# Kernel tuning notes

Measured on AMD Instinct MI355X. Metric: run time of the kernel, lower is better.

## Reference

```python
import jax, jax.numpy as jnp
import numpy as np

WEIGHT = 1e-7       # lambda for the CRF loss
SIGMA_RGB = 15.0    # color-similarity bandwidth
SIGMA_XY = 100.0    # spatial-proximity bandwidth
SCALE = 0.5         # scale_factor (sigma_xy is multiplied by it in forward)


def setup_inputs() -> dict:
    key = jax.random.key(0)
    k1, k2 = jax.random.split(key)
    images = jax.random.uniform(k1, (4, 3, 128, 128), jnp.float32) * 255.0  # [0,255] RGB
    logits = jax.random.normal(k2, (4, 4, 128, 128), jnp.float32)
    segmentations = jax.nn.softmax(logits, axis=1)  # softmaxed logits, N*K*H*W
    return {"images": images, "segmentations": segmentations}


def _crf_loss(images, segmentations):
    n, k, h, w = segmentations.shape
    # F.interpolate(images, scale_factor=0.5, mode='nearest') == stride-2 subsample
    img_s = images[:, :, ::2, ::2]
    # F.interpolate(segs, scale_factor=0.5, mode='bilinear', align_corners=False)
    # for exact /2 downscale == 2x2 average pooling
    hs, ws = h // 2, w // 2
    seg_s = segmentations.reshape(n, k, hs, 2, ws, 2).mean(axis=(3, 5))  # [n,k,hs,ws]

    P = hs * ws
    yy, xx = jnp.meshgrid(jnp.arange(hs, dtype=jnp.float32),
                          jnp.arange(ws, dtype=jnp.float32), indexing='ij')
    sigma_xy_eff = SIGMA_XY * SCALE
    pos = jnp.stack([xx, yy], axis=-1).reshape(P, 2) / sigma_xy_eff      # [P,2]
    rgb = img_s.reshape(n, 3, P).transpose(0, 2, 1) / SIGMA_RGB          # [n,P,3]
    feats = jnp.concatenate([jnp.broadcast_to(pos[None], (n, P, 2)), rgb], axis=-1)  # [n,P,5]

    # exact dense Gaussian bilateral kernel W_ij = exp(-0.5*||f_i - f_j||^2)
    sq = jnp.sum(feats * feats, axis=-1)                                 # [n,P]
    d2 = sq[:, :, None] + sq[:, None, :] - 2.0 * jnp.einsum('npc,nqc->npq', feats, feats)
    Wk = jnp.exp(-0.5 * jnp.maximum(d2, 0.0))                            # [n,P,P]

    S = seg_s.reshape(n, k, P)
    AS = jnp.einsum('npq,nkq->nkp', Wk, S)                               # bilateral-filtered segs
    loss = -jnp.sum(S * AS) / jnp.float32(n)
    return (WEIGHT * loss).reshape(1)


def reference(images, segmentations):
    return _crf_loss(images, segmentations)
```

## Files before the change

kernel.cpp:

```cpp
#include <hip/hip_runtime.h>

#define NB   4
#define KCH  4
#define PPB  4096
#define QT   64
#define BLK  256
#define PT   2
#define NPT  8
#define NBLK 288

#if __has_builtin(__builtin_amdgcn_exp2f)
#define EXPFN(x) __builtin_amdgcn_exp2f(x)
#define FSCALE 1.2011224087864498f
#else
#define EXPFN(x) __expf(x)
#define FSCALE 1.0f
#endif


__global__ __launch_bounds__(256) void crf_prep(const float* __restrict__ images,
                                                const float* __restrict__ segs,
                                                float4* __restrict__ RA,
                                                float4* __restrict__ RB,
                                                float2* __restrict__ RC) {
    int gid = blockIdx.x * BLK + threadIdx.x;
    int n = gid >> 12;
    int p = gid & (PPB - 1);
    int i = p >> 6;
    int j = p & 63;
    int off = 256 * i + 2 * j;
    const float* img = images + (size_t)n * 3 * 16384;
    float x = (float)j * (FSCALE / 50.0f);
    float y = (float)i * (FSCALE / 50.0f);
    float r = img[off]         * (FSCALE / 15.0f);
    float g = img[16384 + off] * (FSCALE / 15.0f);
    float b = img[32768 + off] * (FSCALE / 15.0f);
    float h = -0.5f * (x * x + y * y + r * r + g * g + b * b);
    const float* sg = segs + (size_t)n * KCH * 16384;
    float s0, s1, s2, s3;
    {
        float2 u0 = *(const float2*)(sg + off);
        float2 u1 = *(const float2*)(sg + off + 128);
        s0 = 0.25f * ((u0.x + u0.y) + (u1.x + u1.y));
        u0 = *(const float2*)(sg + 16384 + off);
        u1 = *(const float2*)(sg + 16384 + off + 128);
        s1 = 0.25f * ((u0.x + u0.y) + (u1.x + u1.y));
        u0 = *(const float2*)(sg + 32768 + off);
        u1 = *(const float2*)(sg + 32768 + off + 128);
        s2 = 0.25f * ((u0.x + u0.y) + (u1.x + u1.y));
        u0 = *(const float2*)(sg + 49152 + off);
        u1 = *(const float2*)(sg + 49152 + off + 128);
        s3 = 0.25f * ((u0.x + u0.y) + (u1.x + u1.y));
    }
    RA[gid] = make_float4(x, y, r, g);
    RB[gid] = make_float4(b, h, s0, s1);
    RC[gid] = make_float2(s2, s3);
}

__global__ __launch_bounds__(256) void crf_pairs(const float4* __restrict__ RA,
                                                 const float4* __restrict__ RB,
                                                 const float2* __restrict__ RC,
                                                 float* __restrict__ out) {
    __shared__ float wsum[BLK / 64];
    int t = threadIdx.x;
    int n = blockIdx.y;

    int b = blockIdx.x;
    int pt = 0;
    pt += (b >= 64); pt += (b >= 120); pt += (b >= 168); pt += (b >= 208);
    pt += (b >= 240); pt += (b >= 264); pt += (b >= 280);
    int qc = b - pt * (60 - 4 * pt);
    int pbase = pt * (BLK * PT);
    int qbase = qc * QT;
    bool mixed = (qc >> 3) == pt;
    int base = n << 12;

    float4 a0 = RA[base + pbase + t];
    float4 a1 = RA[base + pbase + t + BLK];
    float4 b0 = RB[base + pbase + t];
    float4 b1 = RB[base + pbase + t + BLK];
    float2 c0 = RC[base + pbase + t];
    float2 c1 = RC[base + pbase + t + BLK];

    const float4* __restrict__ qA = RA + base + qbase;
    const float4* __restrict__ qB = RB + base + qbase;
    const float2* __restrict__ qC = RC + base + qbase;

    float acc0 = 0.f, acc1 = 0.f;
    float acc_all;

    if (!mixed) {
#pragma unroll 4
        for (int q = 0; q < QT; ++q) {
            float4 fa = qA[q];
            float4 fb = qB[q];
            float2 fc = qC[q];
            float d0 = b0.y + fb.y;
            d0 = fmaf(a0.x, fa.x, d0);
            d0 = fmaf(a0.y, fa.y, d0);
            d0 = fmaf(a0.z, fa.z, d0);
            d0 = fmaf(a0.w, fa.w, d0);
            d0 = fmaf(b0.x, fb.x, d0);
            float w0 = EXPFN(d0);
            float sd0 = b0.z * fb.z;
            sd0 = fmaf(b0.w, fb.w, sd0);
            sd0 = fmaf(c0.x, fc.x, sd0);
            sd0 = fmaf(c0.y, fc.y, sd0);
            acc0 = fmaf(w0, sd0, acc0);

            float d1 = b1.y + fb.y;
            d1 = fmaf(a1.x, fa.x, d1);
            d1 = fmaf(a1.y, fa.y, d1);
            d1 = fmaf(a1.z, fa.z, d1);
            d1 = fmaf(a1.w, fa.w, d1);
            d1 = fmaf(b1.x, fb.x, d1);
            float w1 = EXPFN(d1);
            float sd1 = b1.z * fb.z;
            sd1 = fmaf(b1.w, fb.w, sd1);
            sd1 = fmaf(c1.x, fc.x, sd1);
            sd1 = fmaf(c1.y, fc.y, sd1);
            acc1 = fmaf(w1, sd1, acc1);
        }
        acc_all = 2.0f * (acc0 + acc1);
    } else {
        int pg0 = pbase + t;
        int pg1 = pbase + t + BLK;
#pragma unroll 4
        for (int q = 0; q < QT; ++q) {
            float4 fa = qA[q];
            float4 fb = qB[q];
            float2 fc = qC[q];
            int qg = qbase + q;

            float d0 = b0.y + fb.y;
            d0 = fmaf(a0.x, fa.x, d0);
            d0 = fmaf(a0.y, fa.y, d0);
            d0 = fmaf(a0.z, fa.z, d0);
            d0 = fmaf(a0.w, fa.w, d0);
            d0 = fmaf(b0.x, fb.x, d0);
            float w0 = EXPFN(d0);
            float sd0 = b0.z * fb.z;
            sd0 = fmaf(b0.w, fb.w, sd0);
            sd0 = fmaf(c0.x, fc.x, sd0);
            sd0 = fmaf(c0.y, fc.y, sd0);
            float f0 = (qg > pg0) ? 2.0f : ((qg == pg0) ? 1.0f : 0.0f);
            acc0 = fmaf(w0, sd0 * f0, acc0);

            float d1 = b1.y + fb.y;
            d1 = fmaf(a1.x, fa.x, d1);
            d1 = fmaf(a1.y, fa.y, d1);
            d1 = fmaf(a1.z, fa.z, d1);
            d1 = fmaf(a1.w, fa.w, d1);
            d1 = fmaf(b1.x, fb.x, d1);
            float w1 = EXPFN(d1);
            float sd1 = b1.z * fb.z;
            sd1 = fmaf(b1.w, fb.w, sd1);
            sd1 = fmaf(c1.x, fc.x, sd1);
            sd1 = fmaf(c1.y, fc.y, sd1);
            float f1 = (qg > pg1) ? 2.0f : ((qg == pg1) ? 1.0f : 0.0f);
            acc1 = fmaf(w1, sd1 * f1, acc1);
        }
        acc_all = acc0 + acc1;
    }

#pragma unroll
    for (int off = 32; off > 0; off >>= 1)
        acc_all += __shfl_down(acc_all, off, 64);
    if ((t & 63) == 0) wsum[t >> 6] = acc_all;
    __syncthreads();
    if (t == 0) {
        float s = (wsum[0] + wsum[1]) + (wsum[2] + wsum[3]);
        atomicAdd(out, s * (-2.5e-8f));
    }
}

extern "C" void kernel_launch(void* const* d_in, const int* in_sizes, int n_in,
                              void* d_out, int out_size, void* d_ws, size_t ws_size,
                              hipStream_t stream) {
    const float* images = (const float*)d_in[0];
    const float* segs   = (const float*)d_in[1];
    float* out = (float*)d_out;
    char* ws = (char*)d_ws;
    float4* RA = (float4*)(ws);
    float4* RB = (float4*)(ws + 262144);
    float2* RC = (float2*)(ws + 524288);
    (void)in_sizes; (void)n_in; (void)out_size; (void)ws_size;

    (void)hipMemsetAsync(out, 0, sizeof(float), stream);
    crf_prep<<<dim3(64), dim3(256), 0, stream>>>(images, segs, RA, RB, RC);
    crf_pairs<<<dim3(NBLK, NB), dim3(256), 0, stream>>>(RA, RB, RC, out);
}
```

Baseline: 78.90 us.

## Stage q-tile in LDS, raise pixels per thread to four, fold memset into prep

Each thread now holds four p-pixels in registers instead of two. The 64-entry q tile is staged once into shared memory and software-prefetched one step ahead. The triangular block schedule is recomputed for 160 blocks per image, and the separate memset of the output is replaced by a store in the prep kernel. The aims are more work per q-feature load, one fewer launch, and replacing repeated global loads with LDS broadcasts. In exchange there are fewer blocks per image (640 total), which may underfill the GPU, and the four accumulators raise register pressure.

```diff
diff --git a/kernel.cpp b/kernel.cpp
--- a/kernel.cpp
+++ b/kernel.cpp
@@ -5,9 +5,8 @@
 #define PPB  4096
 #define QT   64
 #define BLK  256
-#define PT   2
-#define NPT  8
-#define NBLK 288
+#define PT   4
+#define NBLK 160
 
 #if __has_builtin(__builtin_amdgcn_exp2f)
 #define EXPFN(x) __builtin_amdgcn_exp2f(x)
@@ -22,8 +21,10 @@
                                                 const float* __restrict__ segs,
                                                 float4* __restrict__ RA,
                                                 float4* __restrict__ RB,
-                                                float2* __restrict__ RC) {
+                                                float2* __restrict__ RC,
+                                                float* __restrict__ out) {
     int gid = blockIdx.x * BLK + threadIdx.x;
+    if (gid == 0) out[0] = 0.0f;
     int n = gid >> 12;
     int p = gid & (PPB - 1);
     int i = p >> 6;
@@ -61,106 +62,95 @@
                                                  const float4* __restrict__ RB,
                                                  const float2* __restrict__ RC,
                                                  float* __restrict__ out) {
+    __shared__ float4 ldsA[QT + 1];
+    __shared__ float4 ldsB[QT + 1];
+    __shared__ float2 ldsC[QT + 1];
     __shared__ float wsum[BLK / 64];
+
     int t = threadIdx.x;
     int n = blockIdx.y;
 
     int b = blockIdx.x;
-    int pt = 0;
-    pt += (b >= 64); pt += (b >= 120); pt += (b >= 168); pt += (b >= 208);
-    pt += (b >= 240); pt += (b >= 264); pt += (b >= 280);
-    int qc = b - pt * (60 - 4 * pt);
+    int pt = (b >= 64) + (b >= 112) + (b >= 144);
+    int qc = b - 8 * pt * (7 - pt);
     int pbase = pt * (BLK * PT);
     int qbase = qc * QT;
-    bool mixed = (qc >> 3) == pt;
+    bool mixed = (qc >> 4) == pt;
     int base = n << 12;
 
-    float4 a0 = RA[base + pbase + t];
-    float4 a1 = RA[base + pbase + t + BLK];
-    float4 b0 = RB[base + pbase + t];
-    float4 b1 = RB[base + pbase + t + BLK];
-    float2 c0 = RC[base + pbase + t];
-    float2 c1 = RC[base + pbase + t + BLK];
+    if (t < QT)            ldsA[t]          = RA[base + qbase + t];
+    else if (t < 2 * QT)   ldsB[t - QT]     = RB[base + qbase + (t - QT)];
+    else if (t < 3 * QT)   ldsC[t - 2 * QT] = RC[base + qbase + (t - 2 * QT)];
 
-    const float4* __restrict__ qA = RA + base + qbase;
-    const float4* __restrict__ qB = RB + base + qbase;
-    const float2* __restrict__ qC = RC + base + qbase;
+    float4 pa[PT], pb[PT];
+    float2 pc[PT];
+#pragma unroll
+    for (int pi = 0; pi < PT; ++pi) {
+        int idx = base + pbase + t + pi * BLK;
+        pa[pi] = RA[idx];
+        pb[pi] = RB[idx];
+        pc[pi] = RC[idx];
+    }
+    __syncthreads();
 
-    float acc0 = 0.f, acc1 = 0.f;
+    float acc[PT] = {0.f, 0.f, 0.f, 0.f};
     float acc_all;
 
+    float4 fa = ldsA[0];
+    float4 fb = ldsB[0];
+    float2 fc = ldsC[0];
+
     if (!mixed) {
-#pragma unroll 4
+#pragma unroll 2
         for (int q = 0; q < QT; ++q) {
-            float4 fa = qA[q];
-            float4 fb = qB[q];
-            float2 fc = qC[q];
-            float d0 = b0.y + fb.y;
-            d0 = fmaf(a0.x, fa.x, d0);
-            d0 = fmaf(a0.y, fa.y, d0);
-            d0 = fmaf(a0.z, fa.z, d0);
-            d0 = fmaf(a0.w, fa.w, d0);
-            d0 = fmaf(b0.x, fb.x, d0);
-            float w0 = EXPFN(d0);
-            float sd0 = b0.z * fb.z;
-            sd0 = fmaf(b0.w, fb.w, sd0);
-            sd0 = fmaf(c0.x, fc.x, sd0);
-            sd0 = fmaf(c0.y, fc.y, sd0);
-            acc0 = fmaf(w0, sd0, acc0);
-
-            float d1 = b1.y + fb.y;
-            d1 = fmaf(a1.x, fa.x, d1);
-            d1 = fmaf(a1.y, fa.y, d1);
-            d1 = fmaf(a1.z, fa.z, d1);
-            d1 = fmaf(a1.w, fa.w, d1);
-            d1 = fmaf(b1.x, fb.x, d1);
-            float w1 = EXPFN(d1);
-            float sd1 = b1.z * fb.z;
-            sd1 = fmaf(b1.w, fb.w, sd1);
-            sd1 = fmaf(c1.x, fc.x, sd1);
-            sd1 = fmaf(c1.y, fc.y, sd1);
-            acc1 = fmaf(w1, sd1, acc1);
+            float4 na = ldsA[q + 1];
+            float4 nb = ldsB[q + 1];
+            float2 nc = ldsC[q + 1];
+#pragma unroll
+            for (int pi = 0; pi < PT; ++pi) {
+                float d = pb[pi].y + fb.y;
+                d = fmaf(pa[pi].x, fa.x, d);
+                d = fmaf(pa[pi].y, fa.y, d);
+                d = fmaf(pa[pi].z, fa.z, d);
+                d = fmaf(pa[pi].w, fa.w, d);
+                d = fmaf(pb[pi].x, fb.x, d);
+                float w = EXPFN(d);
+                float sd = pb[pi].z * fb.z;
+                sd = fmaf(pb[pi].w, fb.w, sd);
+                sd = fmaf(pc[pi].x, fc.x, sd);
+                sd = fmaf(pc[pi].y, fc.y, sd);
+                acc[pi] = fmaf(w, sd, acc[pi]);
+            }
+            fa = na; fb = nb; fc = nc;
         }
-        acc_all = 2.0f * (acc0 + acc1);
+        acc_all = 2.0f * ((acc[0] + acc[1]) + (acc[2] + acc[3]));
     } else {
-        int pg0 = pbase + t;
-        int pg1 = pbase + t + BLK;
-#pragma unroll 4
+#pragma unroll 2
         for (int q = 0; q < QT; ++q) {
-            float4 fa = qA[q];
-            float4 fb = qB[q];
-            float2 fc = qC[q];
+            float4 na = ldsA[q + 1];
+            float4 nb = ldsB[q + 1];
+            float2 nc = ldsC[q + 1];
             int qg = qbase + q;
-
-            float d0 = b0.y + fb.y;
-            d0 = fmaf(a0.x, fa.x, d0);
-            d0 = fmaf(a0.y, fa.y, d0);
-            d0 = fmaf(a0.z, fa.z, d0);
-            d0 = fmaf(a0.w, fa.w, d0);
-            d0 = fmaf(b0.x, fb.x, d0);
-            float w0 = EXPFN(d0);
-            float sd0 = b0.z * fb.z;
-            sd0 = fmaf(b0.w, fb.w, sd0);
-            sd0 = fmaf(c0.x, fc.x, sd0);
-            sd0 = fmaf(c0.y, fc.y, sd0);
-            float f0 = (qg > pg0) ? 2.0f : ((qg == pg0) ? 1.0f : 0.0f);
-            acc0 = fmaf(w0, sd0 * f0, acc0);
-
-            float d1 = b1.y + fb.y;
-            d1 = fmaf(a1.x, fa.x, d1);
-            d1 = fmaf(a1.y, fa.y, d1);
-            d1 = fmaf(a1.z, fa.z, d1);
-            d1 = fmaf(a1.w, fa.w, d1);
-            d1 = fmaf(b1.x, fb.x, d1);
-            float w1 = EXPFN(d1);
-            float sd1 = b1.z * fb.z;
-            sd1 = fmaf(b1.w, fb.w, sd1);
-            sd1 = fmaf(c1.x, fc.x, sd1);
-            sd1 = fmaf(c1.y, fc.y, sd1);
-            float f1 = (qg > pg1) ? 2.0f : ((qg == pg1) ? 1.0f : 0.0f);
-            acc1 = fmaf(w1, sd1 * f1, acc1);
+#pragma unroll
+            for (int pi = 0; pi < PT; ++pi) {
+                int pg = pbase + t + pi * BLK;
+                float d = pb[pi].y + fb.y;
+                d = fmaf(pa[pi].x, fa.x, d);
+                d = fmaf(pa[pi].y, fa.y, d);
+                d = fmaf(pa[pi].z, fa.z, d);
+                d = fmaf(pa[pi].w, fa.w, d);
+                d = fmaf(pb[pi].x, fb.x, d);
+                float w = EXPFN(d);
+                float sd = pb[pi].z * fb.z;
+                sd = fmaf(pb[pi].w, fb.w, sd);
+                sd = fmaf(pc[pi].x, fc.x, sd);
+                sd = fmaf(pc[pi].y, fc.y, sd);
+                float f = (qg > pg) ? 2.0f : ((qg == pg) ? 1.0f : 0.0f);
+                acc[pi] = fmaf(w, sd * f, acc[pi]);
+            }
+            fa = na; fb = nb; fc = nc;
         }
-        acc_all = acc0 + acc1;
+        acc_all = (acc[0] + acc[1]) + (acc[2] + acc[3]);
     }
 
 #pragma unroll
@@ -186,7 +176,6 @@
     float2* RC = (float2*)(ws + 524288);
     (void)in_sizes; (void)n_in; (void)out_size; (void)ws_size;
 
-    (void)hipMemsetAsync(out, 0, sizeof(float), stream);
-    crf_prep<<<dim3(64), dim3(256), 0, stream>>>(images, segs, RA, RB, RC);
+    crf_prep<<<dim3(64), dim3(256), 0, stream>>>(images, segs, RA, RB, RC, out);
     crf_pairs<<<dim3(NBLK, NB), dim3(256), 0, stream>>>(RA, RB, RC, out);
 }
```

Measured after the change: 77.78 us. No clear change (-1.4%).

## Halve q-tile, stage q features in LDS, replace atomics with two-pass reduction

Applied to the files above, without the earlier changes.

Cuts the q tile from 64 to 32 so the triangular pair grid has twice as many blocks (576 per image), which spreads the exp-heavy work across more CUs. Each block now stages its q-point features in shared memory instead of reading them from global memory per iteration. The per-block atomicAdd and the memset are replaced by a partial-sum buffer and a separate single-block reduction kernel. This adds one extra kernel launch and a barrier per block.

```diff
diff --git a/kernel.cpp b/kernel.cpp
--- a/kernel.cpp
+++ b/kernel.cpp
@@ -3,11 +3,11 @@
 #define NB   4
 #define KCH  4
 #define PPB  4096
-#define QT   64
+#define QT   32
 #define BLK  256
 #define PT   2
-#define NPT  8
-#define NBLK 288
+#define NBLK 576
+#define NPART (NBLK * NB)
 
 #if __has_builtin(__builtin_amdgcn_exp2f)
 #define EXPFN(x) __builtin_amdgcn_exp2f(x)
@@ -57,34 +57,39 @@
     RC[gid] = make_float2(s2, s3);
 }
 
-__global__ __launch_bounds__(256) void crf_pairs(const float4* __restrict__ RA,
-                                                 const float4* __restrict__ RB,
-                                                 const float2* __restrict__ RC,
-                                                 float* __restrict__ out) {
+__global__ __launch_bounds__(256, 8) void crf_pairs(const float4* __restrict__ RA,
+                                                    const float4* __restrict__ RB,
+                                                    const float2* __restrict__ RC,
+                                                    float* __restrict__ part) {
+    __shared__ float4 ldsA[QT];
+    __shared__ float4 ldsB[QT];
+    __shared__ float2 ldsC[QT];
     __shared__ float wsum[BLK / 64];
+
     int t = threadIdx.x;
     int n = blockIdx.y;
 
     int b = blockIdx.x;
     int pt = 0;
-    pt += (b >= 64); pt += (b >= 120); pt += (b >= 168); pt += (b >= 208);
-    pt += (b >= 240); pt += (b >= 264); pt += (b >= 280);
-    int qc = b - pt * (60 - 4 * pt);
+#pragma unroll
+    for (int i = 1; i < 8; ++i) pt += (b >= 8 * i * (17 - i)) ? 1 : 0;
+    int qc = b - 8 * pt * (17 - pt) + 16 * pt;
     int pbase = pt * (BLK * PT);
     int qbase = qc * QT;
-    bool mixed = (qc >> 3) == pt;
+    bool mixed = (qc >> 4) == pt;
     int base = n << 12;
 
-    float4 a0 = RA[base + pbase + t];
-    float4 a1 = RA[base + pbase + t + BLK];
-    float4 b0 = RB[base + pbase + t];
-    float4 b1 = RB[base + pbase + t + BLK];
-    float2 c0 = RC[base + pbase + t];
-    float2 c1 = RC[base + pbase + t + BLK];
-
-    const float4* __restrict__ qA = RA + base + qbase;
-    const float4* __restrict__ qB = RB + base + qbase;
-    const float2* __restrict__ qC = RC + base + qbase;
+    if (t < QT)            ldsA[t]          = RA[base + qbase + t];
+    else if (t < 2 * QT)   ldsB[t - QT]     = RB[base + qbase + (t - QT)];
+    else if (t < 3 * QT)   ldsC[t - 2 * QT] = RC[base + qbase + (t - 2 * QT)];
+
+    float4 pa0 = RA[base + pbase + t];
+    float4 pa1 = RA[base + pbase + t + BLK];
+    float4 pb0 = RB[base + pbase + t];
+    float4 pb1 = RB[base + pbase + t + BLK];
+    float2 pc0 = RC[base + pbase + t];
+    float2 pc1 = RC[base + pbase + t + BLK];
+    __syncthreads();
 
     float acc0 = 0.f, acc1 = 0.f;
     float acc_all;
@@ -92,33 +97,33 @@
     if (!mixed) {
 #pragma unroll 4
         for (int q = 0; q < QT; ++q) {
-            float4 fa = qA[q];
-            float4 fb = qB[q];
-            float2 fc = qC[q];
-            float d0 = b0.y + fb.y;
-            d0 = fmaf(a0.x, fa.x, d0);
-            d0 = fmaf(a0.y, fa.y, d0);
-            d0 = fmaf(a0.z, fa.z, d0);
-            d0 = fmaf(a0.w, fa.w, d0);
-            d0 = fmaf(b0.x, fb.x, d0);
+            float4 fa = ldsA[q];
+            float4 fb = ldsB[q];
+            float2 fc = ldsC[q];
+            float d0 = pb0.y + fb.y;
+            d0 = fmaf(pa0.x, fa.x, d0);
+            d0 = fmaf(pa0.y, fa.y, d0);
+            d0 = fmaf(pa0.z, fa.z, d0);
+            d0 = fmaf(pa0.w, fa.w, d0);
+            d0 = fmaf(pb0.x, fb.x, d0);
             float w0 = EXPFN(d0);
-            float sd0 = b0.z * fb.z;
-            sd0 = fmaf(b0.w, fb.w, sd0);
-            sd0 = fmaf(c0.x, fc.x, sd0);
-            sd0 = fmaf(c0.y, fc.y, sd0);
+            float sd0 = pb0.z * fb.z;
+            sd0 = fmaf(pb0.w, fb.w, sd0);
+            sd0 = fmaf(pc0.x, fc.x, sd0);
+            sd0 = fmaf(pc0.y, fc.y, sd0);
             acc0 = fmaf(w0, sd0, acc0);
 
-            float d1 = b1.y + fb.y;
-            d1 = fmaf(a1.x, fa.x, d1);
-            d1 = fmaf(a1.y, fa.y, d1);
-            d1 = fmaf(a1.z, fa.z, d1);
-            d1 = fmaf(a1.w, fa.w, d1);
-            d1 = fmaf(b1.x, fb.x, d1);
+            float d1 = pb1.y + fb.y;
+            d1 = fmaf(pa1.x, fa.x, d1);
+            d1 = fmaf(pa1.y, fa.y, d1);
+            d1 = fmaf(pa1.z, fa.z, d1);
+            d1 = fmaf(pa1.w, fa.w, d1);
+            d1 = fmaf(pb1.x, fb.x, d1);
             float w1 = EXPFN(d1);
-            float sd1 = b1.z * fb.z;
-            sd1 = fmaf(b1.w, fb.w, sd1);
-            sd1 = fmaf(c1.x, fc.x, sd1);
-            sd1 = fmaf(c1.y, fc.y, sd1);
+            float sd1 = pb1.z * fb.z;
+            sd1 = fmaf(pb1.w, fb.w, sd1);
+            sd1 = fmaf(pc1.x, fc.x, sd1);
+            sd1 = fmaf(pc1.y, fc.y, sd1);
             acc1 = fmaf(w1, sd1, acc1);
         }
         acc_all = 2.0f * (acc0 + acc1);
@@ -127,36 +132,35 @@
         int pg1 = pbase + t + BLK;
 #pragma unroll 4
         for (int q = 0; q < QT; ++q) {
-            float4 fa = qA[q];
-            float4 fb = qB[q];
-            float2 fc = qC[q];
+            float4 fa = ldsA[q];
+            float4 fb = ldsB[q];
+            float2 fc = ldsC[q];
             int qg = qbase + q;
-
-            float d0 = b0.y + fb.y;
-            d0 = fmaf(a0.x, fa.x, d0);
-            d0 = fmaf(a0.y, fa.y, d0);
-            d0 = fmaf(a0.z, fa.z, d0);
-            d0 = fmaf(a0.w, fa.w, d0);
-            d0 = fmaf(b0.x, fb.x, d0);
+            float d0 = pb0.y + fb.y;
+            d0 = fmaf(pa0.x, fa.x, d0);
+            d0 = fmaf(pa0.y, fa.y, d0);
+            d0 = fmaf(pa0.z, fa.z, d0);
+            d0 = fmaf(pa0.w, fa.w, d0);
+            d0 = fmaf(pb0.x, fb.x, d0);
             float w0 = EXPFN(d0);
-            float sd0 = b0.z * fb.z;
-            sd0 = fmaf(b0.w, fb.w, sd0);
-            sd0 = fmaf(c0.x, fc.x, sd0);
-            sd0 = fmaf(c0.y, fc.y, sd0);
+            float sd0 = pb0.z * fb.z;
+            sd0 = fmaf(pb0.w, fb.w, sd0);
+            sd0 = fmaf(pc0.x, fc.x, sd0);
+            sd0 = fmaf(pc0.y, fc.y, sd0);
             float f0 = (qg > pg0) ? 2.0f : ((qg == pg0) ? 1.0f : 0.0f);
             acc0 = fmaf(w0, sd0 * f0, acc0);
 
-            float d1 = b1.y + fb.y;
-            d1 = fmaf(a1.x, fa.x, d1);
-            d1 = fmaf(a1.y, fa.y, d1);
-            d1 = fmaf(a1.z, fa.z, d1);
-            d1 = fmaf(a1.w, fa.w, d1);
-            d1 = fmaf(b1.x, fb.x, d1);
+            float d1 = pb1.y + fb.y;
+            d1 = fmaf(pa1.x, fa.x, d1);
+            d1 = fmaf(pa1.y, fa.y, d1);
+            d1 = fmaf(pa1.z, fa.z, d1);
+            d1 = fmaf(pa1.w, fa.w, d1);
+            d1 = fmaf(pb1.x, fb.x, d1);
             float w1 = EXPFN(d1);
-            float sd1 = b1.z * fb.z;
-            sd1 = fmaf(b1.w, fb.w, sd1);
-            sd1 = fmaf(c1.x, fc.x, sd1);
-            sd1 = fmaf(c1.y, fc.y, sd1);
+            float sd1 = pb1.z * fb.z;
+            sd1 = fmaf(pb1.w, fb.w, sd1);
+            sd1 = fmaf(pc1.x, fc.x, sd1);
+            sd1 = fmaf(pc1.y, fc.y, sd1);
             float f1 = (qg > pg1) ? 2.0f : ((qg == pg1) ? 1.0f : 0.0f);
             acc1 = fmaf(w1, sd1 * f1, acc1);
         }
@@ -169,8 +173,27 @@
     if ((t & 63) == 0) wsum[t >> 6] = acc_all;
     __syncthreads();
     if (t == 0) {
-        float s = (wsum[0] + wsum[1]) + (wsum[2] + wsum[3]);
-        atomicAdd(out, s * (-2.5e-8f));
+        part[n * NBLK + blockIdx.x] =
+            (wsum[0] + wsum[1]) + (wsum[2] + wsum[3]);
+    }
+}
+
+__global__ __launch_bounds__(256) void crf_reduce(const float* __restrict__ part,
+                                                  float* __restrict__ out) {
+    __shared__ float wsum[BLK / 64];
+    int t = threadIdx.x;
+    float s = 0.f;
+#pragma unroll
+    for (int i = 0; i < NPART / BLK; ++i)
+        s += part[t + i * BLK];
+#pragma unroll
+    for (int off = 32; off > 0; off >>= 1)
+        s += __shfl_down(s, off, 64);
+    if ((t & 63) == 0) wsum[t >> 6] = s;
+    __syncthreads();
+    if (t == 0) {
+        float tot = (wsum[0] + wsum[1]) + (wsum[2] + wsum[3]);
+        out[0] = tot * (-2.5e-8f);
     }
 }
 
@@ -184,9 +207,10 @@
     float4* RA = (float4*)(ws);
     float4* RB = (float4*)(ws + 262144);
     float2* RC = (float2*)(ws + 524288);
+    float* part = (float*)(ws + 655360);
     (void)in_sizes; (void)n_in; (void)out_size; (void)ws_size;
 
-    (void)hipMemsetAsync(out, 0, sizeof(float), stream);
     crf_prep<<<dim3(64), dim3(256), 0, stream>>>(images, segs, RA, RB, RC);
-    crf_pairs<<<dim3(NBLK, NB), dim3(256), 0, stream>>>(RA, RB, RC, out);
-}
+    crf_pairs<<<dim3(NBLK, NB), dim3(256), 0, stream>>>(RA, RB, RC, part);
+    crf_reduce<<<dim3(1), dim3(256), 0, stream>>>(part, out);
+}
```

Measured after the change: 74.23 us (median of 2 runs). 5.9% less time.
